# Kernel optimization log

Measured on AMD Instinct MI355X. Metric: run time of the kernel, lower is better.

The kernel has to match this reference:

```python
import jax, jax.numpy as jnp
import numpy as np

ALPHA = 4.0  # spikingjelly default Sigmoid surrogate alpha
BN_EPS = 1e-5

@jax.custom_vjp
def _spike(v):
    return (v >= 0.0).astype(v.dtype)

def _spike_fwd(v):
    return _spike(v), v

def _spike_bwd(v, g):
    s = jax.nn.sigmoid(ALPHA * v)
    return (g * ALPHA * s * (1.0 - s),)

_spike.defvjp(_spike_fwd, _spike_bwd)

def lif(x, v_th):
    # Single-step LIFNode(tau=2, v_reset=0) starting from v=0:
    # v = v + (x - v)/tau = x/2 ; spike = Heaviside(v - v_th)
    return _spike(x * 0.5 - v_th)

def bn(x, p):
    # p: [4, C] = gamma, beta, running_mean, running_var (inference BN)
    g, b, m, v = p
    scale = g * jax.lax.rsqrt(v + BN_EPS)
    return x * scale[None, :, None, None] + (b - m * scale)[None, :, None, None]

def conv1x1(x, w):
    # x: [B,C,H,W], w: [O,C]
    return jnp.einsum('bchw,oc->bohw', x, w)

def dwconv3x3(x, w):
    # depthwise 3x3, w: [C,3,3]
    C = x.shape[1]
    return jax.lax.conv_general_dilated(
        x, w[:, None], (1, 1), 'SAME',
        feature_group_count=C,
        dimension_numbers=('NCHW', 'OIHW', 'NCHW'))

def branch(x, w1, dw, w2, bns):
    # RepConv: conv1x1 -> BN -> (dw3x3 -> pw1x1 -> BN), then the extra Sequential BN
    x = bn(conv1x1(x, w1), bns[0])
    x = bn(conv1x1(dwconv3x3(x, dw), w2), bns[1])
    return bn(x, bns[2])

def setup_inputs() -> dict:
    key = jax.random.key(0)
    ks = jax.random.split(key, 5)
    B, C, H, W = 16, 256, 80, 80
    x = jax.random.normal(ks[0], (B, C, H, W), jnp.float32) * 2.0  # so LIFs actually fire
    w1 = jax.random.normal(ks[1], (4, C, C), jnp.float32) * 0.06
    dw = jax.random.normal(ks[2], (4, C, 3, 3), jnp.float32) * 0.3
    w2 = jax.random.normal(ks[3], (4, C, C), jnp.float32) * 0.06
    bn_params = jax.random.uniform(ks[4], (4, 3, 4, C), jnp.float32, 0.1, 1.0)
    return {"x": x, "w1": w1, "dw": dw, "w2": w2, "bn_params": bn_params}

def reference(x, w1, dw, w2, bn_params):
    scale = 0.125
    xs = lif(x, 1.0)                                   # head_lif
    q = branch(xs, w1[0], dw[0], w2[0], bn_params[0])  # q_conv (q_lif unused in source)
    k = branch(xs, w1[1], dw[1], w2[1], bn_params[1])  # k_conv (k_lif unused in source)
    v = branch(xs, w1[2], dw[2], w2[2], bn_params[2])  # v_conv
    v = lif(v, 1.0)                                    # v_lif -> binary spikes
    # k.transpose(-2,-1) @ v : per (b,c) [W,H] @ [H,W] -> [W,W]
    kv = jnp.einsum('bchw,bchu->bcwu', k, v)
    # q @ kv : [H,W] @ [W,W] -> [H,W]
    attn = jnp.einsum('bchw,bcwu->bchu', q, kv) * scale
    s = lif(attn, 0.5)                                 # attn_lif, v_threshold=0.5
    return branch(s, w1[3], dw[3], w2[3], bn_params[3])  # proj_conv
```

## Files before the change

kernel.cpp:

```cpp
#include <hip/hip_runtime.h>
#include <hip/hip_bf16.h>
#include <cstdint>
#include <cstddef>
#include <cmath>

typedef unsigned short u16;
typedef unsigned char  u8;
typedef unsigned int   u32;
typedef __attribute__((ext_vector_type(8))) short short8;
typedef __attribute__((ext_vector_type(4))) float f32x4;
typedef __attribute__((ext_vector_type(4))) u16 u16x4;

#define CCH 256
#define HWP 6400

__device__ __forceinline__ u16 f2bf(float f) {
  u32 u = __float_as_uint(f);
  u = (u + 0x7FFFu + ((u >> 16) & 1u)) >> 16;
  return (u16)u;
}
__device__ __forceinline__ float bf2f(u16 h) { return __uint_as_float(((u32)h) << 16); }
__device__ __forceinline__ void split3(float v, u16& h, u16& m, u16& l) {
  h = f2bf(v); float r = v - bf2f(h);
  m = f2bf(r); l = f2bf(r - bf2f(m));
}
__device__ __forceinline__ void gl_lds16(const void* g, void* l) {
  __builtin_amdgcn_global_load_lds((const __attribute__((address_space(1))) unsigned int*)g,
                                   (__attribute__((address_space(3))) unsigned int*)l,
                                   16, 0, 0);
}

__global__ __launch_bounds__(256) void fold_weights(
    const float* __restrict__ w1, const float* __restrict__ w2,
    const float* __restrict__ bnp,
    u16* __restrict__ w1h, u16* __restrict__ w1m, u16* __restrict__ w1l,
    u16* __restrict__ w2h, u16* __restrict__ w2m, u16* __restrict__ w2l,
    float* __restrict__ b0f, float* __restrict__ b2f)
{
  int i = blockIdx.x >> 8, o = blockIdx.x & 255, c = threadIdx.x;
  const float* bp = bnp + i * 3072;
  double g0 = bp[0 + o],    be0 = bp[256 + o],  m0 = bp[512 + o],  v0 = bp[768 + o];
  double g1 = bp[1024 + o], be1 = bp[1280 + o], m1 = bp[1536 + o], v1 = bp[1792 + o];
  double g2 = bp[2048 + o], be2 = bp[2304 + o], m2 = bp[2560 + o], v2 = bp[2816 + o];
  double s0 = g0 / sqrt(v0 + 1e-5);
  double s1 = g1 / sqrt(v1 + 1e-5);
  double s2 = g2 / sqrt(v2 + 1e-5);
  size_t ro = (size_t)(i * 256 + o) * 256;
  float wa = (float)(s0 * (double)w1[ro + c]);
  float wb = (float)(s1 * s2 * (double)w2[ro + c]);
  u16 h, m, l;
  split3(wa, h, m, l); w1h[ro + c] = h; w1m[ro + c] = m; w1l[ro + c] = l;
  split3(wb, h, m, l); w2h[ro + c] = h; w2m[ro + c] = m; w2l[ro + c] = l;
  if (c == 0) {
    b0f[i * 256 + o] = (float)(be0 - m0 * s0);
    b2f[i * 256 + o] = (float)(s2 * (be1 - m1 * s1) + be2 - m2 * s2);
  }
}

__global__ __launch_bounds__(256) void head_spike(
    const float* __restrict__ x, u8* __restrict__ xs, int b0)
{
  __shared__ u8 tile[64][68];
  int z = blockIdx.z, c0 = blockIdx.y << 6, p0 = blockIdx.x << 6;
  int tid = threadIdx.x;
  const float* xb = x + ((size_t)(b0 + z) * CCH + c0) * HWP + p0;
#pragma unroll
  for (int j = 0; j < 16; ++j) {
    int idx = j * 256 + tid;
    int cl = idx >> 6, pl = idx & 63;
    tile[pl][cl] = (xb[(size_t)cl * HWP + pl] >= 2.0f) ? 1 : 0;
  }
  __syncthreads();
#pragma unroll
  for (int j = 0; j < 4; ++j) {
    int idx = j * 256 + tid;
    int row = idx >> 4, c4 = (idx & 15) << 2;
    *(uchar4*)(xs + ((size_t)z * HWP + p0 + row) * CCH + c0 + c4) =
        *(const uchar4*)&tile[row][c4];
  }
}

__global__ __launch_bounds__(256) void transpose_s(
    const u8* __restrict__ in, u8* __restrict__ out, int b0)
{
  __shared__ u8 tile[64][68];
  int z = blockIdx.z, c0 = blockIdx.y << 6, p0 = blockIdx.x << 6;
  int tid = threadIdx.x;
#pragma unroll
  for (int j = 0; j < 4; ++j) {
    int idx = j * 256 + tid;
    int cl = idx >> 4, p4 = (idx & 15) << 2;
    uchar4 v = *(const uchar4*)(in + ((size_t)z * CCH + c0 + cl) * HWP + p0 + p4);
    tile[p4 + 0][cl] = v.x; tile[p4 + 1][cl] = v.y;
    tile[p4 + 2][cl] = v.z; tile[p4 + 3][cl] = v.w;
  }
  __syncthreads();
#pragma unroll
  for (int j = 0; j < 4; ++j) {
    int idx = j * 256 + tid;
    int row = idx >> 4, c4 = (idx & 15) << 2;
    *(uchar4*)(out + ((size_t)(b0 + z) * HWP + p0 + row) * CCH + c0 + c4) =
        *(const uchar4*)&tile[row][c4];
  }
}

__global__ __launch_bounds__(256, 4) void gemm1(
    const u8* __restrict__ act, int b0in,
    const u16* __restrict__ WH, const u16* __restrict__ WM, const u16* __restrict__ WL,
    const float* __restrict__ bias, float* __restrict__ T1)
{
  __shared__ alignas(16) u16 As[128 * 40];
  __shared__ alignas(16) u16 LWH[4096];
  __shared__ alignas(16) u16 LWM[4096];
  __shared__ alignas(16) u16 LWL[4096];
  const int tid = threadIdx.x, wave = tid >> 6, lane = tid & 63;
  const int p0 = blockIdx.x * 128, o0 = blockIdx.y * 128, z = blockIdx.z;
  const int wm = (wave >> 1) * 64, wn = (wave & 1) * 64;
  const int lc = lane & 15, lr = lane >> 4;
  const u8* ab = act + ((size_t)(b0in + z) * HWP + p0) * CCH;
  const char* whb = (const char*)(WH + (size_t)o0 * 256);
  const char* wmb = (const char*)(WM + (size_t)o0 * 256);
  const char* wlb = (const char*)(WL + (size_t)o0 * 256);

  f32x4 acc[4][4];
#pragma unroll
  for (int i = 0; i < 4; ++i)
#pragma unroll
    for (int j = 0; j < 4; ++j) acc[i][j] = (f32x4){0.f, 0.f, 0.f, 0.f};

  const int srow = tid >> 1, shalf = tid & 1;

  for (int kc = 0; kc < 8; ++kc) {
    const int kof = kc * 64;
    __syncthreads();
#pragma unroll
    for (int t = 0; t < 2; ++t) {
      int li = t * 256 + tid;
      int row = li >> 2, ch = li & 3;
      int chp = (ch - row - (row >> 2)) & 3;
      size_t so = (size_t)row * 512 + kof + chp * 16;
      int base = (t * 256 + wave * 64) * 8;
      gl_lds16(whb + so, &LWH[base]);
      gl_lds16(wmb + so, &LWM[base]);
      gl_lds16(wlb + so, &LWL[base]);
    }
    uint4 u = *(const uint4*)(ab + (size_t)srow * CCH + kc * 32 + shalf * 16);
    u32 vv[4] = {u.x, u.y, u.z, u.w};
    u32 w[8];
#pragma unroll
    for (int q = 0; q < 4; ++q) {
      u32 v = vv[q];
      w[2 * q]     = ((v & 255u) ? 0x3F80u : 0u) | (((v >> 8) & 255u) ? 0x3F800000u : 0u);
      w[2 * q + 1] = (((v >> 16) & 255u) ? 0x3F80u : 0u) | (((v >> 24) & 255u) ? 0x3F800000u : 0u);
    }
    *(uint4*)&As[srow * 40 + shalf * 16]     = (uint4){w[0], w[1], w[2], w[3]};
    *(uint4*)&As[srow * 40 + shalf * 16 + 8] = (uint4){w[4], w[5], w[6], w[7]};
    __syncthreads();
    short8 af[4];
#pragma unroll
    for (int i = 0; i < 4; ++i)
      af[i] = *(const short8*)&As[(wm + i * 16 + lc) * 40 + lr * 8];
#pragma unroll
    for (int j = 0; j < 4; ++j) {
      int row = wn + j * 16 + lc;
      int o = row * 32 + ((lr + lc + (lc >> 2)) & 3) * 8;
      short8 bh = *(const short8*)&LWH[o];
      short8 bm = *(const short8*)&LWM[o];
      short8 bl = *(const short8*)&LWL[o];
#pragma unroll
      for (int i = 0; i < 4; ++i) {
        acc[i][j] = __builtin_amdgcn_mfma_f32_16x16x32_bf16(af[i], bl, acc[i][j], 0, 0, 0);
        acc[i][j] = __builtin_amdgcn_mfma_f32_16x16x32_bf16(af[i], bm, acc[i][j], 0, 0, 0);
        acc[i][j] = __builtin_amdgcn_mfma_f32_16x16x32_bf16(af[i], bh, acc[i][j], 0, 0, 0);
      }
    }
  }
  float* tb = T1 + ((size_t)z * HWP + p0) * CCH + o0;
#pragma unroll
  for (int j = 0; j < 4; ++j) {
    int n = wn + j * 16 + lc;
    float bn_ = bias[o0 + n];
#pragma unroll
    for (int i = 0; i < 4; ++i) {
      int m = wm + i * 16 + lr * 4;
#pragma unroll
      for (int r = 0; r < 4; ++r)
        tb[(size_t)(m + r) * CCH + n] = acc[i][j][r] + bn_;
    }
  }
}

__global__ __launch_bounds__(256) void dw3(
    const float* __restrict__ t1, const float* __restrict__ dwk,
    u16* __restrict__ oh, u16* __restrict__ om, u16* __restrict__ ol)
{
  __shared__ float wl[2304];
  int tid = threadIdx.x;
#pragma unroll
  for (int t = 0; t < 9; ++t) wl[t * 256 + tid] = dwk[t * 256 + tid];
  int c4 = (tid & 63) << 2;
  int pl = tid >> 6;
  int p = blockIdx.x * 4 + pl;
  int z = blockIdx.y;
  int y = p / 80, x = p - y * 80;
  __syncthreads();
  float a0 = 0.f, a1 = 0.f, a2 = 0.f, a3 = 0.f;
  const float* base = t1 + (size_t)z * HWP * CCH;
  const float* wc = &wl[c4 * 9];
#pragma unroll
  for (int dy = -1; dy <= 1; ++dy) {
    int yy = y + dy;
    bool vy = (unsigned)yy < 80u;
#pragma unroll
    for (int dx = -1; dx <= 1; ++dx) {
      int xx = x + dx;
      if (vy && (unsigned)xx < 80u) {
        float4 v = *(const float4*)(base + (size_t)(yy * 80 + xx) * CCH + c4);
        int t = (dy + 1) * 3 + (dx + 1);
        a0 += wc[t]      * v.x;
        a1 += wc[9 + t]  * v.y;
        a2 += wc[18 + t] * v.z;
        a3 += wc[27 + t] * v.w;
      }
    }
  }
  u16 h0, m0, l0, h1, m1, l1, h2, m2, l2, h3, m3, l3;
  split3(a0, h0, m0, l0);
  split3(a1, h1, m1, l1);
  split3(a2, h2, m2, l2);
  split3(a3, h3, m3, l3);
  u16x4 vh, vm, vlo;
  vh.x = h0; vh.y = h1; vh.z = h2; vh.w = h3;
  vm.x = m0; vm.y = m1; vm.z = m2; vm.w = m3;
  vlo.x = l0; vlo.y = l1; vlo.z = l2; vlo.w = l3;
  size_t addr = ((size_t)z * HWP + p) * CCH + c4;
  *(u16x4*)(oh + addr) = vh;
  *(u16x4*)(om + addr) = vm;
  *(u16x4*)(ol + addr) = vlo;
}

template <int MODE>
__global__ __launch_bounds__(256) void gemm2s(
    const u16* __restrict__ AH, const u16* __restrict__ AM, const u16* __restrict__ AL,
    const u16* __restrict__ WH, const u16* __restrict__ WM, const u16* __restrict__ WL,
    const float* __restrict__ bias, int b0,
    float* __restrict__ outF, u8* __restrict__ outB,
    u16* __restrict__ outH, u16* __restrict__ outM, u16* __restrict__ outL)
{
  __shared__ alignas(16) u16 LAH[4096];
  __shared__ alignas(16) u16 LAM[4096];
  __shared__ alignas(16) u16 LAL[4096];
  __shared__ alignas(16) u16 LWH[4096];
  __shared__ alignas(16) u16 LWM[4096];
  __shared__ alignas(16) u16 LWL[4096];
  const int tid = threadIdx.x, wave = tid >> 6, lane = tid & 63;
  const int p0 = blockIdx.x * 128, o0 = blockIdx.y * 128, z = blockIdx.z;
  const int wm = (wave >> 1) * 64, wn = (wave & 1) * 64;
  const int lc = lane & 15, lr = lane >> 4;
  const char* ahb = (const char*)(AH + ((size_t)z * HWP + p0) * 256);
  const char* amb = (const char*)(AM + ((size_t)z * HWP + p0) * 256);
  const char* alb = (const char*)(AL + ((size_t)z * HWP + p0) * 256);
  const char* whb = (const char*)(WH + (size_t)o0 * 256);
  const char* wmb = (const char*)(WM + (size_t)o0 * 256);
  const char* wlb = (const char*)(WL + (size_t)o0 * 256);

  f32x4 acc[4][4];
#pragma unroll
  for (int i = 0; i < 4; ++i)
#pragma unroll
    for (int j = 0; j < 4; ++j) acc[i][j] = (f32x4){0.f, 0.f, 0.f, 0.f};

  for (int kc = 0; kc < 8; ++kc) {
    const int kof = kc * 64;
#pragma unroll
    for (int t = 0; t < 2; ++t) {
      int li = t * 256 + tid;
      int row = li >> 2, ch = li & 3;
      int chp = (ch - row - (row >> 2)) & 3;
      size_t so = (size_t)row * 512 + kof + chp * 16;
      int base = (t * 256 + wave * 64) * 8;
      gl_lds16(ahb + so, &LAH[base]);
      gl_lds16(amb + so, &LAM[base]);
      gl_lds16(alb + so, &LAL[base]);
      gl_lds16(whb + so, &LWH[base]);
      gl_lds16(wmb + so, &LWM[base]);
      gl_lds16(wlb + so, &LWL[base]);
    }
    __syncthreads();
    short8 afH[4], afM[4], afL[4];
#pragma unroll
    for (int i = 0; i < 4; ++i) {
      int row = wm + i * 16 + lc;
      int o = row * 32 + ((lr + lc + (lc >> 2)) & 3) * 8;
      afH[i] = *(const short8*)&LAH[o];
      afM[i] = *(const short8*)&LAM[o];
      afL[i] = *(const short8*)&LAL[o];
    }
#pragma unroll
    for (int j = 0; j < 4; ++j) {
      int row = wn + j * 16 + lc;
      int o = row * 32 + ((lr + lc + (lc >> 2)) & 3) * 8;
      short8 bh = *(const short8*)&LWH[o];
      short8 bm = *(const short8*)&LWM[o];
      short8 bl = *(const short8*)&LWL[o];
#pragma unroll
      for (int i = 0; i < 4; ++i) {
        acc[i][j] = __builtin_amdgcn_mfma_f32_16x16x32_bf16(afM[i], bm, acc[i][j], 0, 0, 0);
        acc[i][j] = __builtin_amdgcn_mfma_f32_16x16x32_bf16(afL[i], bh, acc[i][j], 0, 0, 0);
        acc[i][j] = __builtin_amdgcn_mfma_f32_16x16x32_bf16(afH[i], bl, acc[i][j], 0, 0, 0);
        acc[i][j] = __builtin_amdgcn_mfma_f32_16x16x32_bf16(afM[i], bh, acc[i][j], 0, 0, 0);
        acc[i][j] = __builtin_amdgcn_mfma_f32_16x16x32_bf16(afH[i], bm, acc[i][j], 0, 0, 0);
        acc[i][j] = __builtin_amdgcn_mfma_f32_16x16x32_bf16(afH[i], bh, acc[i][j], 0, 0, 0);
      }
    }
    __syncthreads();
  }
#pragma unroll
  for (int j = 0; j < 4; ++j) {
    int n = o0 + wn + j * 16 + lc;
    float bn_ = bias[n];
    size_t rowb = ((size_t)(b0 + z) * CCH + n) * HWP + p0;
#pragma unroll
    for (int i = 0; i < 4; ++i) {
      int m = wm + i * 16 + lr * 4;
      if (MODE == 0) {
        float4 o;
        o.x = acc[i][j][0] + bn_; o.y = acc[i][j][1] + bn_;
        o.z = acc[i][j][2] + bn_; o.w = acc[i][j][3] + bn_;
        *(float4*)(outF + rowb + m) = o;
      } else if (MODE == 1) {
        uchar4 o;
        o.x = (acc[i][j][0] + bn_ >= 2.0f) ? 1 : 0;
        o.y = (acc[i][j][1] + bn_ >= 2.0f) ? 1 : 0;
        o.z = (acc[i][j][2] + bn_ >= 2.0f) ? 1 : 0;
        o.w = (acc[i][j][3] + bn_ >= 2.0f) ? 1 : 0;
        *(uchar4*)(outB + rowb + m) = o;
      } else {
        u16x4 vh, vm2, vl2;
#pragma unroll
        for (int r = 0; r < 4; ++r) {
          u16 hh, mm, ll;
          split3(acc[i][j][r] + bn_, hh, mm, ll);
          vh[r] = hh; vm2[r] = mm; vl2[r] = ll;
        }
        *(u16x4*)(outH + rowb + m) = vh;
        *(u16x4*)(outM + rowb + m) = vm2;
        *(u16x4*)(outL + rowb + m) = vl2;
      }
    }
  }
}

__global__ __launch_bounds__(320) void attn_k(
    const u16* __restrict__ qh_g, const u16* __restrict__ qm_g, const u16* __restrict__ ql_g,
    const u16* __restrict__ kh_g, const u16* __restrict__ km_g, const u16* __restrict__ kl_g,
    const u8* __restrict__ vv, u8* __restrict__ s)
{
  __shared__ alignas(16) u16 L[24960];
  __shared__ alignas(16) u8  VT[8320];
  const int tid = threadIdx.x, wave = tid >> 6, lane = tid & 63;
  const int lc = lane & 15, lr = lane >> 4;
  const size_t off = (size_t)blockIdx.x * HWP;
  u16* KH = L; u16* KM = L + 8320; u16* KL = L + 16640;

  short8 qfr[3][3];
  const int hrow = wave * 16 + lc;
#pragma unroll
  for (int kc = 0; kc < 3; ++kc) {
    int w0 = kc * 32 + lr * 8;
    if (w0 < 80) {
      size_t qo = off + (size_t)hrow * 80 + w0;
      qfr[kc][0] = *(const short8*)(qh_g + qo);
      qfr[kc][1] = *(const short8*)(qm_g + qo);
      qfr[kc][2] = *(const short8*)(ql_g + qo);
    } else {
      qfr[kc][0] = (short8){0, 0, 0, 0, 0, 0, 0, 0};
      qfr[kc][1] = qfr[kc][0];
      qfr[kc][2] = qfr[kc][0];
    }
  }

#pragma unroll
  for (int t = 0; t < 3; ++t) {
    int g = t * 320 + tid;
    int h = g / 12, wc = g - h * 12;
    int dst = h * 104 + wc * 8;
    if (wc < 10) {
      size_t so = off + (size_t)h * 80 + wc * 8;
      *(short8*)&KH[dst] = *(const short8*)(kh_g + so);
      *(short8*)&KM[dst] = *(const short8*)(km_g + so);
      *(short8*)&KL[dst] = *(const short8*)(kl_g + so);
    } else {
      short8 z8 = (short8){0, 0, 0, 0, 0, 0, 0, 0};
      *(short8*)&KH[dst] = z8; *(short8*)&KM[dst] = z8; *(short8*)&KL[dst] = z8;
    }
  }
  {
    int row = tid >> 2, qq = tid & 3;
    *(u32*)&VT[row * 104 + 80 + qq * 4] = 0;
  }
#pragma unroll
  for (int t = 0; t < 5; ++t) {
    int q = t * 320 + tid;
    int h = q / 20, w4 = (q - h * 20) * 4;
    uchar4 v4 = *(const uchar4*)(vv + off + (size_t)h * 80 + w4);
    VT[(w4 + 0) * 104 + h] = v4.x;
    VT[(w4 + 1) * 104 + h] = v4.y;
    VT[(w4 + 2) * 104 + h] = v4.z;
    VT[(w4 + 3) * 104 + h] = v4.w;
  }
  __syncthreads();

  f32x4 accS[5];
#pragma unroll
  for (int n = 0; n < 5; ++n) accS[n] = (f32x4){0.f, 0.f, 0.f, 0.f};
  for (int kc = 0; kc < 3; ++kc) {
#pragma unroll
    for (int n = 0; n < 5; ++n) {
      int bo = (n * 16 + lc) * 104 + kc * 32 + lr * 8;
      short8 kh_ = *(const short8*)&KH[bo];
      short8 km_ = *(const short8*)&KM[bo];
      short8 kl_ = *(const short8*)&KL[bo];
      __builtin_amdgcn_s_setprio(1);
      accS[n] = __builtin_amdgcn_mfma_f32_16x16x32_bf16(qfr[kc][0], kl_, accS[n], 0, 0, 0);
      accS[n] = __builtin_amdgcn_mfma_f32_16x16x32_bf16(qfr[kc][2], kh_, accS[n], 0, 0, 0);
      accS[n] = __builtin_amdgcn_mfma_f32_16x16x32_bf16(qfr[kc][1], km_, accS[n], 0, 0, 0);
      accS[n] = __builtin_amdgcn_mfma_f32_16x16x32_bf16(qfr[kc][1], kh_, accS[n], 0, 0, 0);
      accS[n] = __builtin_amdgcn_mfma_f32_16x16x32_bf16(qfr[kc][0], km_, accS[n], 0, 0, 0);
      accS[n] = __builtin_amdgcn_mfma_f32_16x16x32_bf16(qfr[kc][0], kh_, accS[n], 0, 0, 0);
      __builtin_amdgcn_s_setprio(0);
    }
  }
  __syncthreads();
#pragma unroll
  for (int n = 0; n < 5; ++n) {
#pragma unroll
    for (int r = 0; r < 4; ++r) {
      u16 hh, mm, ll; split3(accS[n][r], hh, mm, ll);
      int o = (wave * 16 + lr * 4 + r) * 104 + n * 16 + lc;
      KH[o] = hh; KM[o] = mm; KL[o] = ll;
    }
  }
  __syncthreads();
  f32x4 accA[5];
#pragma unroll
  for (int n = 0; n < 5; ++n) accA[n] = (f32x4){0.f, 0.f, 0.f, 0.f};
  for (int kc = 0; kc < 3; ++kc) {
    int ao = (wave * 16 + lc) * 104 + kc * 32 + lr * 8;
    short8 sh_ = *(const short8*)&KH[ao];
    short8 sm_ = *(const short8*)&KM[ao];
    short8 sl_ = *(const short8*)&KL[ao];
#pragma unroll
    for (int n = 0; n < 5; ++n) {
      const u8* vp = &VT[(n * 16 + lc) * 104 + kc * 32 + lr * 8];
      u32 b0 = *(const u32*)vp;
      u32 b1 = *(const u32*)(vp + 4);
      u32 e0 = ((b0 & 255u) ? 0x3F80u : 0u) | (((b0 >> 8) & 255u) ? 0x3F800000u : 0u);
      u32 e1 = (((b0 >> 16) & 255u) ? 0x3F80u : 0u) | (((b0 >> 24) & 255u) ? 0x3F800000u : 0u);
      u32 e2 = ((b1 & 255u) ? 0x3F80u : 0u) | (((b1 >> 8) & 255u) ? 0x3F800000u : 0u);
      u32 e3 = (((b1 >> 16) & 255u) ? 0x3F80u : 0u) | (((b1 >> 24) & 255u) ? 0x3F800000u : 0u);
      u32 vbw[4] = {e0, e1, e2, e3};
      short8 vb = *(const short8*)vbw;
      __builtin_amdgcn_s_setprio(1);
      accA[n] = __builtin_amdgcn_mfma_f32_16x16x32_bf16(sl_, vb, accA[n], 0, 0, 0);
      accA[n] = __builtin_amdgcn_mfma_f32_16x16x32_bf16(sm_, vb, accA[n], 0, 0, 0);
      accA[n] = __builtin_amdgcn_mfma_f32_16x16x32_bf16(sh_, vb, accA[n], 0, 0, 0);
      __builtin_amdgcn_s_setprio(0);
    }
  }
#pragma unroll
  for (int n = 0; n < 5; ++n)
#pragma unroll
    for (int r = 0; r < 4; ++r)
      s[off + (size_t)(wave * 16 + lr * 4 + r) * 80 + n * 16 + lc] =
          (accA[n][r] >= 8.0f) ? 1 : 0;
}

extern "C" void kernel_launch(void* const* d_in, const int* in_sizes, int n_in,
                              void* d_out, int out_size, void* d_ws, size_t ws_size,
                              hipStream_t stream)
{
  const float* x   = (const float*)d_in[0];
  const float* w1  = (const float*)d_in[1];
  const float* dwk = (const float*)d_in[2];
  const float* w2  = (const float*)d_in[3];
  const float* bnp = (const float*)d_in[4];
  float* out = (float*)d_out;
  char* ws = (char*)d_ws;

  u16* W1H = (u16*)(ws + 0);
  u16* W1M = (u16*)(ws + 524288);
  u16* W1L = (u16*)(ws + 1048576);
  u16* W2H = (u16*)(ws + 1572864);
  u16* W2M = (u16*)(ws + 2097152);
  u16* W2L = (u16*)(ws + 2621440);
  float* B0F = (float*)(ws + 3145728);
  float* B2F = (float*)(ws + 3149824);
  u8*    SPM = (u8*)(ws + 3153920);
  u8*    XS  = (u8*)(ws + 29368320);
  float* T1  = (float*)(ws + 42475520);
  u16*   KH_ = (u16*)(ws + 42475520);
  u16*   KM_ = (u16*)(ws + 68689920);
  u16*   QH_ = (u16*)(ws + 94904320);
  u16*   QM_ = (u16*)(ws + 121118720);
  u16*   QL_ = (u16*)(ws + 147333120);
  u16*   KL_ = (u16*)(ws + 173547520);
  u8*    V   = (u8*)(ws + 199761920);
  u16*   D2H = (u16*)(ws + 212869120);
  u16*   D2M = (u16*)(ws + 239083520);
  u16*   D2L = (u16*)(ws + 265297920);

  dim3 gb(256);
  fold_weights<<<dim3(1024), gb, 0, stream>>>(w1, w2, bnp,
      W1H, W1M, W1L, W2H, W2M, W2L, B0F, B2F);

  for (int c = 0; c < 2; ++c) {
    int b0 = c * 8;
    dim3 gh(100, 4, 8), gg(50, 2, 8), gd(1600, 8);
    head_spike<<<gh, gb, 0, stream>>>(x, XS, b0);
    gemm1<<<gg, gb, 0, stream>>>(XS, 0, W1H + 2 * 65536, W1M + 2 * 65536, W1L + 2 * 65536,
                                 B0F + 512, T1);
    dw3<<<gd, gb, 0, stream>>>(T1, dwk + 2 * 2304, D2H, D2M, D2L);
    gemm2s<1><<<gg, gb, 0, stream>>>(D2H, D2M, D2L,
                                     W2H + 2 * 65536, W2M + 2 * 65536, W2L + 2 * 65536,
                                     B2F + 512, 0, nullptr, V, nullptr, nullptr, nullptr);
    gemm1<<<gg, gb, 0, stream>>>(XS, 0, W1H + 0 * 65536, W1M + 0 * 65536, W1L + 0 * 65536,
                                 B0F + 0, T1);
    dw3<<<gd, gb, 0, stream>>>(T1, dwk + 0 * 2304, D2H, D2M, D2L);
    gemm2s<2><<<gg, gb, 0, stream>>>(D2H, D2M, D2L,
                                     W2H + 0 * 65536, W2M + 0 * 65536, W2L + 0 * 65536,
                                     B2F + 0, 0, nullptr, nullptr, QH_, QM_, QL_);
    gemm1<<<gg, gb, 0, stream>>>(XS, 0, W1H + 1 * 65536, W1M + 1 * 65536, W1L + 1 * 65536,
                                 B0F + 256, T1);
    dw3<<<gd, gb, 0, stream>>>(T1, dwk + 1 * 2304, D2H, D2M, D2L);
    gemm2s<2><<<gg, gb, 0, stream>>>(D2H, D2M, D2L,
                                     W2H + 1 * 65536, W2M + 1 * 65536, W2L + 1 * 65536,
                                     B2F + 256, 0, nullptr, nullptr, KH_, KM_, KL_);
    attn_k<<<dim3(2048), dim3(320), 0, stream>>>(QH_, QM_, QL_, KH_, KM_, KL_, V, V);
    transpose_s<<<gh, gb, 0, stream>>>(V, SPM, b0);
  }
  for (int c = 0; c < 2; ++c) {
    int b0 = c * 8;
    dim3 gg(50, 2, 8), gd(1600, 8);
    gemm1<<<gg, gb, 0, stream>>>(SPM, b0, W1H + 3 * 65536, W1M + 3 * 65536, W1L + 3 * 65536,
                                 B0F + 768, T1);
    dw3<<<gd, gb, 0, stream>>>(T1, dwk + 3 * 2304, D2H, D2M, D2L);
    gemm2s<0><<<gg, gb, 0, stream>>>(D2H, D2M, D2L,
                                     W2H + 3 * 65536, W2M + 3 * 65536, W2L + 3 * 65536,
                                     B2F + 768, b0, out, nullptr, nullptr, nullptr, nullptr);
  }
}
```

Before: 1.385 ms.

## Widen gemm2s tile to all 256 output channels with 512-thread blocks

The gemm2s kernel now computes a 128-pixel by 256-channel tile per block using 8 waves instead of 128x128 with 4 waves, so each A tile (three bf16 split planes) is loaded from global memory once rather than twice. Grid drops from (50,2,8) to (50,8), and LDS for weights doubles to hold 256 rows. This halves A-operand traffic but reduces block count and raises LDS use per block, which may lower occupancy; the k-loop is also marked not unrolled.

```diff
diff --git a/kernel.cpp b/kernel.cpp
--- a/kernel.cpp
+++ b/kernel.cpp
@@ -240,7 +240,7 @@
 }
 
 template <int MODE>
-__global__ __launch_bounds__(256) void gemm2s(
+__global__ __launch_bounds__(512, 4) void gemm2s(
     const u16* __restrict__ AH, const u16* __restrict__ AM, const u16* __restrict__ AL,
     const u16* __restrict__ WH, const u16* __restrict__ WM, const u16* __restrict__ WL,
     const float* __restrict__ bias, int b0,
@@ -250,19 +250,19 @@
   __shared__ alignas(16) u16 LAH[4096];
   __shared__ alignas(16) u16 LAM[4096];
   __shared__ alignas(16) u16 LAL[4096];
-  __shared__ alignas(16) u16 LWH[4096];
-  __shared__ alignas(16) u16 LWM[4096];
-  __shared__ alignas(16) u16 LWL[4096];
+  __shared__ alignas(16) u16 LWH[8192];
+  __shared__ alignas(16) u16 LWM[8192];
+  __shared__ alignas(16) u16 LWL[8192];
   const int tid = threadIdx.x, wave = tid >> 6, lane = tid & 63;
-  const int p0 = blockIdx.x * 128, o0 = blockIdx.y * 128, z = blockIdx.z;
-  const int wm = (wave >> 1) * 64, wn = (wave & 1) * 64;
+  const int p0 = blockIdx.x * 128, z = blockIdx.y;
+  const int wm = (wave >> 2) * 64, wn = (wave & 3) * 64;
   const int lc = lane & 15, lr = lane >> 4;
   const char* ahb = (const char*)(AH + ((size_t)z * HWP + p0) * 256);
   const char* amb = (const char*)(AM + ((size_t)z * HWP + p0) * 256);
   const char* alb = (const char*)(AL + ((size_t)z * HWP + p0) * 256);
-  const char* whb = (const char*)(WH + (size_t)o0 * 256);
-  const char* wmb = (const char*)(WM + (size_t)o0 * 256);
-  const char* wlb = (const char*)(WL + (size_t)o0 * 256);
+  const char* whb = (const char*)WH;
+  const char* wmb = (const char*)WM;
+  const char* wlb = (const char*)WL;
 
   f32x4 acc[4][4];
 #pragma unroll
@@ -270,18 +270,26 @@
 #pragma unroll
     for (int j = 0; j < 4; ++j) acc[i][j] = (f32x4){0.f, 0.f, 0.f, 0.f};
 
+#pragma unroll 1
   for (int kc = 0; kc < 8; ++kc) {
     const int kof = kc * 64;
-#pragma unroll
-    for (int t = 0; t < 2; ++t) {
-      int li = t * 256 + tid;
+    {
+      int li = tid;
       int row = li >> 2, ch = li & 3;
       int chp = (ch - row - (row >> 2)) & 3;
       size_t so = (size_t)row * 512 + kof + chp * 16;
-      int base = (t * 256 + wave * 64) * 8;
+      int base = wave * 512;
       gl_lds16(ahb + so, &LAH[base]);
       gl_lds16(amb + so, &LAM[base]);
       gl_lds16(alb + so, &LAL[base]);
+    }
+#pragma unroll
+    for (int t = 0; t < 2; ++t) {
+      int li = t * 512 + tid;
+      int row = li >> 2, ch = li & 3;
+      int chp = (ch - row - (row >> 2)) & 3;
+      size_t so = (size_t)row * 512 + kof + chp * 16;
+      int base = t * 4096 + wave * 512;
       gl_lds16(whb + so, &LWH[base]);
       gl_lds16(wmb + so, &LWM[base]);
       gl_lds16(wlb + so, &LWL[base]);
@@ -317,7 +325,7 @@
   }
 #pragma unroll
   for (int j = 0; j < 4; ++j) {
-    int n = o0 + wn + j * 16 + lc;
+    int n = wn + j * 16 + lc;
     float bn_ = bias[n];
     size_t rowb = ((size_t)(b0 + z) * CCH + n) * HWP + p0;
 #pragma unroll
@@ -516,24 +524,24 @@
 
   for (int c = 0; c < 2; ++c) {
     int b0 = c * 8;
-    dim3 gh(100, 4, 8), gg(50, 2, 8), gd(1600, 8);
+    dim3 gh(100, 4, 8), gg(50, 2, 8), gg2(50, 8), gd(1600, 8);
     head_spike<<<gh, gb, 0, stream>>>(x, XS, b0);
     gemm1<<<gg, gb, 0, stream>>>(XS, 0, W1H + 2 * 65536, W1M + 2 * 65536, W1L + 2 * 65536,
                                  B0F + 512, T1);
     dw3<<<gd, gb, 0, stream>>>(T1, dwk + 2 * 2304, D2H, D2M, D2L);
-    gemm2s<1><<<gg, gb, 0, stream>>>(D2H, D2M, D2L,
+    gemm2s<1><<<gg2, dim3(512), 0, stream>>>(D2H, D2M, D2L,
                                      W2H + 2 * 65536, W2M + 2 * 65536, W2L + 2 * 65536,
                                      B2F + 512, 0, nullptr, V, nullptr, nullptr, nullptr);
     gemm1<<<gg, gb, 0, stream>>>(XS, 0, W1H + 0 * 65536, W1M + 0 * 65536, W1L + 0 * 65536,
                                  B0F + 0, T1);
     dw3<<<gd, gb, 0, stream>>>(T1, dwk + 0 * 2304, D2H, D2M, D2L);
-    gemm2s<2><<<gg, gb, 0, stream>>>(D2H, D2M, D2L,
+    gemm2s<2><<<gg2, dim3(512), 0, stream>>>(D2H, D2M, D2L,
                                      W2H + 0 * 65536, W2M + 0 * 65536, W2L + 0 * 65536,
                                      B2F + 0, 0, nullptr, nullptr, QH_, QM_, QL_);
     gemm1<<<gg, gb, 0, stream>>>(XS, 0, W1H + 1 * 65536, W1M + 1 * 65536, W1L + 1 * 65536,
                                  B0F + 256, T1);
     dw3<<<gd, gb, 0, stream>>>(T1, dwk + 1 * 2304, D2H, D2M, D2L);
-    gemm2s<2><<<gg, gb, 0, stream>>>(D2H, D2M, D2L,
+    gemm2s<2><<<gg2, dim3(512), 0, stream>>>(D2H, D2M, D2L,
                                      W2H + 1 * 65536, W2M + 1 * 65536, W2L + 1 * 65536,
                                      B2F + 256, 0, nullptr, nullptr, KH_, KM_, KL_);
     attn_k<<<dim3(2048), dim3(320), 0, stream>>>(QH_, QM_, QL_, KH_, KM_, KL_, V, V);
@@ -541,11 +549,11 @@
   }
   for (int c = 0; c < 2; ++c) {
     int b0 = c * 8;
-    dim3 gg(50, 2, 8), gd(1600, 8);
+    dim3 gg(50, 2, 8), gg2(50, 8), gd(1600, 8);
     gemm1<<<gg, gb, 0, stream>>>(SPM, b0, W1H + 3 * 65536, W1M + 3 * 65536, W1L + 3 * 65536,
                                  B0F + 768, T1);
     dw3<<<gd, gb, 0, stream>>>(T1, dwk + 3 * 2304, D2H, D2M, D2L);
-    gemm2s<0><<<gg, gb, 0, stream>>>(D2H, D2M, D2L,
+    gemm2s<0><<<gg2, dim3(512), 0, stream>>>(D2H, D2M, D2L,
                                      W2H + 3 * 65536, W2M + 3 * 65536, W2L + 3 * 65536,
                                      B2F + 768, b0, out, nullptr, nullptr, nullptr, nullptr);
   }
```

After: 1.601 ms. 15.6% more time.
